# Performance work log

Measured on AMD Instinct MI355X. Metric: run time of the kernel, lower is better.

Reference implementation:

```python
import jax, jax.numpy as jnp
import numpy as np

BEAM_WIDTH = 5  # degenerate: all beams share the same per-step topk, so best beam == greedy argmax path
BLANK = 0


def setup_inputs() -> dict:
    key = jax.random.key(0)
    N, C, T = 128, 128, 2048
    logits = jax.random.normal(key, (N, C, T), dtype=jnp.float32)
    return {"logits": logits}


def reference(logits) -> jnp.ndarray:
    # (N, C, T) -> (N, T, C), log-softmax over classes (matches F.log_softmax(dim=2))
    log_probs = jax.nn.log_softmax(jnp.transpose(logits, (0, 2, 1)), axis=2)
    N, T, C = log_probs.shape
    # Beam search in the source is degenerate: every beam expands with the identical
    # per-timestep top-k, so the highest-scoring beam is exactly the per-step argmax.
    tokens = jnp.argmax(log_probs, axis=2).astype(jnp.int32)  # (N, T)
    # CTC-style collapse (decode()): drop blanks and repeated tokens.
    prev = jnp.concatenate([jnp.full((N, 1), -1, dtype=jnp.int32), tokens[:, :-1]], axis=1)
    keep = (tokens != BLANK) & (tokens != prev)  # (N, T) bool
    # Left-compact kept tokens into a blank-padded (N, T) output.
    pos = jnp.cumsum(keep, axis=1) - 1            # target position if kept
    pos = jnp.where(keep, pos, T)                 # dropped tokens -> dump slot T
    out = jnp.full((N, T + 1), BLANK, dtype=jnp.int32)
    out = out.at[jnp.arange(N)[:, None], pos].set(tokens)
    return out[:, :T]
```

## Files before the change

### kernel.cpp

```cpp
#include <hip/hip_runtime.h>


constexpr int N = 128;
constexpr int C = 128;
constexpr int T = 2048;

__global__ __launch_bounds__(256) void argmax_kernel(const float* __restrict__ logits,
                                                     int* __restrict__ tokens) {
    __shared__ float sb[3][4][64];
    __shared__ int   si[3][4][64];

    const int tid = threadIdx.x;
    const int tq  = tid & 63;
    const int grp = tid >> 6;
    const int b   = blockIdx.x;
    const int n   = b & 127;
    const int t4  = (b >> 7) * 256 + tq * 4;

    const float* base = logits + (size_t)n * C * T + (size_t)(grp * 32) * T + t4;

    float4 best = make_float4(-__builtin_inff(), -__builtin_inff(),
                              -__builtin_inff(), -__builtin_inff());
    int4 bidx = make_int4(0, 0, 0, 0);

    #pragma unroll
    for (int cc = 0; cc < 32; cc += 8) {
        float4 v[8];
        #pragma unroll
        for (int j = 0; j < 8; ++j)
            v[j] = *(const float4*)(base + (size_t)(cc + j) * T);
        #pragma unroll
        for (int j = 0; j < 8; ++j) {
            const int c = cc + j;
            if (v[j].x > best.x) { best.x = v[j].x; bidx.x = c; }
            if (v[j].y > best.y) { best.y = v[j].y; bidx.y = c; }
            if (v[j].z > best.z) { best.z = v[j].z; bidx.z = c; }
            if (v[j].w > best.w) { best.w = v[j].w; bidx.w = c; }
        }
    }

    if (grp > 0) {
        sb[grp - 1][0][tq] = best.x; si[grp - 1][0][tq] = bidx.x + grp * 32;
        sb[grp - 1][1][tq] = best.y; si[grp - 1][1][tq] = bidx.y + grp * 32;
        sb[grp - 1][2][tq] = best.z; si[grp - 1][2][tq] = bidx.z + grp * 32;
        sb[grp - 1][3][tq] = best.w; si[grp - 1][3][tq] = bidx.w + grp * 32;
    }
    __syncthreads();
    if (grp == 0) {
        #pragma unroll
        for (int g = 0; g < 3; ++g) {
            float f;
            f = sb[g][0][tq]; if (f > best.x) { best.x = f; bidx.x = si[g][0][tq]; }
            f = sb[g][1][tq]; if (f > best.y) { best.y = f; bidx.y = si[g][1][tq]; }
            f = sb[g][2][tq]; if (f > best.z) { best.z = f; bidx.z = si[g][2][tq]; }
            f = sb[g][3][tq]; if (f > best.w) { best.w = f; bidx.w = si[g][3][tq]; }
        }
        *(int4*)(tokens + (size_t)n * T + t4) = bidx;
    }
}

__global__ __launch_bounds__(256) void collapse_kernel(const int* __restrict__ tokens,
                                                       int* __restrict__ out) {
    const int n = blockIdx.x;
    const int* trow = tokens + (size_t)n * T;
    int* orow = out + (size_t)n * T;
    const int tid = threadIdx.x;
    constexpr int PER = T / 256;
    const int t0 = tid * PER;

    int tok[PER];
    *(int4*)&tok[0] = *(const int4*)(trow + t0);
    *(int4*)&tok[4] = *(const int4*)(trow + t0 + 4);
    int prev = (t0 == 0) ? -1 : trow[t0 - 1];

    int kpos[PER];
    int cnt = 0;
    #pragma unroll
    for (int i = 0; i < PER; ++i) {
        const bool k = (tok[i] != 0) && (tok[i] != prev);
        kpos[i] = k ? cnt : -1;
        cnt += k ? 1 : 0;
        prev = tok[i];
    }

    const int lane = tid & 63;
    const int wid  = tid >> 6;
    int incl = cnt;
    #pragma unroll
    for (int d = 1; d < 64; d <<= 1) {
        int v = __shfl_up(incl, d, 64);
        if (lane >= d) incl += v;
    }

    __shared__ int wsum[4];
    if (lane == 63) wsum[wid] = incl;

    const int4 z = make_int4(0, 0, 0, 0);
    *(int4*)(orow + t0)     = z;
    *(int4*)(orow + t0 + 4) = z;

    __syncthreads();

    int wbase = 0;
    #pragma unroll
    for (int w = 0; w < 4; ++w)
        if (w < wid) wbase += wsum[w];
    const int base2 = wbase + (incl - cnt);

    #pragma unroll
    for (int i = 0; i < PER; ++i) {
        if (kpos[i] >= 0) orow[base2 + kpos[i]] = tok[i];
    }
}

extern "C" void kernel_launch(void* const* d_in, const int* in_sizes, int n_in,
                              void* d_out, int out_size, void* d_ws, size_t ws_size,
                              hipStream_t stream) {
    const float* logits = (const float*)d_in[0];
    int* out = (int*)d_out;
    int* tokens = (int*)d_ws;

    argmax_kernel<<<N * 8, 256, 0, stream>>>(logits, tokens);
    collapse_kernel<<<N, 256, 0, stream>>>(tokens, out);
}
```

Baseline: 29.26 us.

## Spread argmax reduction across all warps and move output zeroing into argmax kernel

The final cross-group argmax reduction now runs on all four wavefronts: each thread handles one (timestep, component) pair instead of only wavefront 0 doing it. Zero-filling of the output row moves from the collapse kernel into the argmax kernel. Block-to-(n, chunk) mapping changes so consecutive blocks cover the same batch row. This shortens the serial tail of the argmax kernel and the store work in the small, latency-bound collapse kernel, at the cost of scalar rather than vector token stores.

```diff
diff --git a/kernel.cpp b/kernel.cpp
--- a/kernel.cpp
+++ b/kernel.cpp
@@ -6,16 +6,18 @@
 constexpr int T = 2048;
 
 __global__ __launch_bounds__(256) void argmax_kernel(const float* __restrict__ logits,
-                                                     int* __restrict__ tokens) {
-    __shared__ float sb[3][4][64];
-    __shared__ int   si[3][4][64];
+                                                     int* __restrict__ tokens,
+                                                     int* __restrict__ out) {
+    __shared__ float sb[4][64][4];
+    __shared__ int   si[4][64][4];
 
-    const int tid = threadIdx.x;
-    const int tq  = tid & 63;
-    const int grp = tid >> 6;
-    const int b   = blockIdx.x;
-    const int n   = b & 127;
-    const int t4  = (b >> 7) * 256 + tq * 4;
+    const int tid   = threadIdx.x;
+    const int tq    = tid & 63;
+    const int grp   = tid >> 6;
+    const int b     = blockIdx.x;
+    const int n     = b >> 3;
+    const int chunk = b & 7;
+    const int t4    = chunk * 256 + tq * 4;
 
     const float* base = logits + (size_t)n * C * T + (size_t)(grp * 32) * T + t4;
 
@@ -39,24 +41,25 @@
         }
     }
 
-    if (grp > 0) {
-        sb[grp - 1][0][tq] = best.x; si[grp - 1][0][tq] = bidx.x + grp * 32;
-        sb[grp - 1][1][tq] = best.y; si[grp - 1][1][tq] = bidx.y + grp * 32;
-        sb[grp - 1][2][tq] = best.z; si[grp - 1][2][tq] = bidx.z + grp * 32;
-        sb[grp - 1][3][tq] = best.w; si[grp - 1][3][tq] = bidx.w + grp * 32;
+    *(float4*)sb[grp][tq] = best;
+    int4 gi = make_int4(bidx.x + grp * 32, bidx.y + grp * 32,
+                        bidx.z + grp * 32, bidx.w + grp * 32);
+    *(int4*)si[grp][tq] = gi;
+
+    out[(size_t)n * T + chunk * 256 + tid] = 0;
+
+    __syncthreads();
+
+    const int comp = tid & 3;
+    const int q    = tid >> 2;
+    float fb = sb[0][q][comp];
+    int   ib = si[0][q][comp];
+    #pragma unroll
+    for (int g = 1; g < 4; ++g) {
+        const float f = sb[g][q][comp];
+        if (f > fb) { fb = f; ib = si[g][q][comp]; }
     }
-    __syncthreads();
-    if (grp == 0) {
-        #pragma unroll
-        for (int g = 0; g < 3; ++g) {
-            float f;
-            f = sb[g][0][tq]; if (f > best.x) { best.x = f; bidx.x = si[g][0][tq]; }
-            f = sb[g][1][tq]; if (f > best.y) { best.y = f; bidx.y = si[g][1][tq]; }
-            f = sb[g][2][tq]; if (f > best.z) { best.z = f; bidx.z = si[g][2][tq]; }
-            f = sb[g][3][tq]; if (f > best.w) { best.w = f; bidx.w = si[g][3][tq]; }
-        }
-        *(int4*)(tokens + (size_t)n * T + t4) = bidx;
-    }
+    tokens[(size_t)n * T + chunk * 256 + tid] = ib;
 }
 
 __global__ __launch_bounds__(256) void collapse_kernel(const int* __restrict__ tokens,
@@ -94,11 +97,6 @@
 
     __shared__ int wsum[4];
     if (lane == 63) wsum[wid] = incl;
-
-    const int4 z = make_int4(0, 0, 0, 0);
-    *(int4*)(orow + t0)     = z;
-    *(int4*)(orow + t0 + 4) = z;
-
     __syncthreads();
 
     int wbase = 0;
@@ -120,6 +118,6 @@
     int* out = (int*)d_out;
     int* tokens = (int*)d_ws;
 
-    argmax_kernel<<<N * 8, 256, 0, stream>>>(logits, tokens);
+    argmax_kernel<<<N * 8, 256, 0, stream>>>(logits, tokens, out);
     collapse_kernel<<<N, 256, 0, stream>>>(tokens, out);
 }
```

Measured after the change: 27.63 us. -5.6%, faster.
